# Kernel tuning notes

Measured on AMD Instinct MI355X. Metric: run time of the kernel, lower is better.

The kernel has to match this reference:

```python
import jax, jax.numpy as jnp
import numpy as np

B, C, H, W = 512, 2048, 8, 6
NATTR = 51
HID = 128
EPS = 1e-5


def setup_inputs() -> dict:
    key = jax.random.key(0)
    ks = jax.random.split(key, 12)
    inp = {
        "x_body_feat": jax.random.normal(ks[0], (B, C, H, W), dtype=jnp.float32),
        "x_face_feat": jax.random.normal(ks[1], (B, C, H, W), dtype=jnp.float32),
        "pose": jax.random.randint(ks[2], (B,), 0, 2, dtype=jnp.int64),
        "A_front": jax.random.normal(ks[3], (C, H, W), dtype=jnp.float32),
        # w1 MLP: Linear(2048->128), ReLU, Linear(128->2048), Sigmoid
        "W1": jax.random.normal(ks[4], (HID, C), dtype=jnp.float32) * (1.0 / np.sqrt(C)),
        "b1": jnp.zeros((HID,), dtype=jnp.float32),
        "W2": jax.random.normal(ks[5], (C, HID), dtype=jnp.float32) * (1.0 / np.sqrt(HID)),
        "b2": jnp.zeros((C,), dtype=jnp.float32),
        # logits: Linear(2048->nattr) + BatchNorm1d(nattr)
        "Wl": jax.random.normal(ks[6], (NATTR, C), dtype=jnp.float32) * (1.0 / np.sqrt(C)),
        "bl": jnp.zeros((NATTR,), dtype=jnp.float32),
        "gamma": jnp.ones((NATTR,), dtype=jnp.float32),
        "beta": jnp.zeros((NATTR,), dtype=jnp.float32),
    }
    return inp


def reference(x_body_feat, x_face_feat, pose, A_front, W1, b1, W2, b2, Wl, bl, gamma, beta):
    # Vectorized, mask-based form of the per-sample loop in A_operation.
    # comb_feat = body * A_front * face  -> [B, C, H, W]
    comb = x_body_feat * A_front[None] * x_face_feat
    # w1: MaxPool2d((8,6)) over full spatial extent -> [B, C], then MLP
    pooled = jnp.max(comb, axis=(2, 3))
    h = jax.nn.relu(pooled @ W1.T + b1)            # [B, 128]
    gate = jax.nn.sigmoid(h @ W2.T + b2)            # [B, 2048]
    cand = x_body_feat + gate[:, :, None, None]     # broadcast add, [B,C,H,W]
    # pose == 1 -> gated branch, else passthrough body features
    front = (pose == 1)[:, None, None, None]
    feat = jnp.where(front, cand, x_body_feat)
    # AdaptiveAvgPool2d(1) -> global mean
    gap = jnp.mean(feat, axis=(2, 3))               # [B, 2048]
    z = gap @ Wl.T + bl                             # [B, nattr]
    # BatchNorm1d in training mode: batch statistics (biased variance)
    mu = jnp.mean(z, axis=0)
    var = jnp.mean((z - mu) ** 2, axis=0)
    return gamma * (z - mu) * jax.lax.rsqrt(var + EPS) + beta
```

## Files before the change

### kernel.cpp

```cpp
#include <hip/hip_runtime.h>
#include <hip/hip_bf16.h>
#include <math.h>

#define B_    512
#define C_    2048
#define HW_   48
#define HID_  128
#define NATTR_ 51
#define EPS_  1e-5f

__global__ __launch_bounds__(256) void fused_pool(
    const float* __restrict__ body, const float* __restrict__ face,
    const float* __restrict__ A, float* __restrict__ pooled,
    float* __restrict__ bmean) {
  __shared__ float smax[256 * 13];
  __shared__ float ssum[256 * 13];
  const int t = threadIdx.x;
  const int base_f4 = blockIdx.x * 3072;
  const int cb12 = (blockIdx.x & 7) * 3072;
  const float4* __restrict__ b4 = (const float4*)body;
  const float4* __restrict__ f4 = (const float4*)face;
  const float4* __restrict__ a4 = (const float4*)A;
#pragma unroll
  for (int half = 0; half < 2; ++half) {
    float4 vb[6], vf[6], va[6];
#pragma unroll
    for (int j = 0; j < 6; ++j) {
      const int fl = t + 256 * (half * 6 + j);
      vb[j] = b4[base_f4 + fl];
      vf[j] = f4[base_f4 + fl];
      va[j] = a4[cb12 + fl];
    }
#pragma unroll
    for (int j = 0; j < 6; ++j) {
      const int fl = t + 256 * (half * 6 + j);
      const int rl = fl / 12, p = fl % 12;
      const float m0 = vb[j].x * va[j].x * vf[j].x;
      const float m1 = vb[j].y * va[j].y * vf[j].y;
      const float m2 = vb[j].z * va[j].z * vf[j].z;
      const float m3 = vb[j].w * va[j].w * vf[j].w;
      smax[rl * 13 + p] = fmaxf(fmaxf(m0, m1), fmaxf(m2, m3));
      ssum[rl * 13 + p] = (vb[j].x + vb[j].y) + (vb[j].z + vb[j].w);
    }
  }
  __syncthreads();
  float m = -INFINITY, s = 0.f;
#pragma unroll
  for (int p = 0; p < 12; ++p) {
    m = fmaxf(m, smax[t * 13 + p]);
    s += ssum[t * 13 + p];
  }
  const int row = blockIdx.x * 256 + t;
  pooled[row] = m;
  bmean[row] = s * (1.0f / 48.0f);
}

__global__ __launch_bounds__(256) void mlp1(
    const float* __restrict__ pooled, const float* __restrict__ W1,
    const float* __restrict__ b1, float* __restrict__ h) {
  const int t = threadIdx.x;
  const int lane = t & 63;
  const int w = t >> 6;
  const int sg = blockIdx.x >> 2;
  const int og = (blockIdx.x & 3) * 4 + w;
  const int s0 = sg * 8, o0 = og * 8;
  float acc[8][8] = {};
  const float* __restrict__ pb = pooled + lane;
  const float* __restrict__ wb = W1 + lane;
  for (int kc = 0; kc < 32; ++kc) {
    const int k = kc * 64;
    float p[8], wv[8];
#pragma unroll
    for (int i = 0; i < 8; ++i) p[i] = pb[(s0 + i) * C_ + k];
#pragma unroll
    for (int j = 0; j < 8; ++j) wv[j] = wb[(o0 + j) * C_ + k];
#pragma unroll
    for (int i = 0; i < 8; ++i)
#pragma unroll
      for (int j = 0; j < 8; ++j) acc[i][j] += p[i] * wv[j];
  }
#pragma unroll
  for (int d = 32; d >= 1; d >>= 1)
#pragma unroll
    for (int i = 0; i < 8; ++i)
#pragma unroll
      for (int j = 0; j < 8; ++j) acc[i][j] += __shfl_down(acc[i][j], d);
  if (lane == 0) {
#pragma unroll
    for (int i = 0; i < 8; ++i)
#pragma unroll
      for (int j = 0; j < 8; ++j)
        h[(s0 + i) * HID_ + o0 + j] = fmaxf(acc[i][j] + b1[o0 + j], 0.f);
  }
}

__global__ __launch_bounds__(256) void mlp2(
    const float* __restrict__ h, const float* __restrict__ W2,
    const float* __restrict__ b2, const float* __restrict__ bmean,
    const int* __restrict__ pose, float* __restrict__ gap) {
  extern __shared__ float w2s[];
  const int t = threadIdx.x;
  const int ct = blockIdx.x & 15, st = blockIdx.x >> 4;
  const int c0 = ct * 128, s_base = st * 32;
  const float4* __restrict__ wg = (const float4*)(W2 + c0 * HID_);
#pragma unroll
  for (int r = 0; r < 16; ++r) {
    const int f = t + 256 * r;
    const int row = f >> 5, col4 = f & 31;
    *(float4*)&w2s[row * 144 + col4 * 4] = wg[f];
  }
  __syncthreads();
  const int c_l = t & 127, sh = t >> 7;
  const int c = c0 + c_l;
  const float bias = b2[c];
  const float* __restrict__ wrow = &w2s[c_l * 144];
  for (int si = 0; si < 16; ++si) {
    const int s = s_base + sh * 16 + si;
    const float fr = (pose[s] == 1) ? 1.f : 0.f;
    float a0 = 0.f, a1 = 0.f, a2 = 0.f, a3 = 0.f;
#pragma unroll
    for (int j = 0; j < 32; ++j) {
      const float4 hv = *(const float4*)&h[s * HID_ + 4 * j];
      const float4 wv = *(const float4*)&wrow[4 * j];
      a0 += hv.x * wv.x;
      a1 += hv.y * wv.y;
      a2 += hv.z * wv.z;
      a3 += hv.w * wv.w;
    }
    const float acc = (a0 + a1) + (a2 + a3);
    const float g = 1.f / (1.f + expf(-(acc + bias)));
    gap[s * C_ + c] = bmean[s * C_ + c] + fr * g;
  }
}

__global__ __launch_bounds__(256) void logits_k(
    const float* __restrict__ gap, const float* __restrict__ Wl,
    const float* __restrict__ bl, float* __restrict__ z) {
  const int t = threadIdx.x;
  const int lane = t & 63;
  const int w = t >> 6;
  const int s0 = blockIdx.x * 4;
  const int o0 = w * 16;
  float acc[4][16] = {};
  const float* __restrict__ gb = gap + lane;
  const float* __restrict__ wb = Wl + lane;
  for (int kc = 0; kc < 32; ++kc) {
    const int k = kc * 64;
    float p[4], wv[16];
#pragma unroll
    for (int i = 0; i < 4; ++i) p[i] = gb[(s0 + i) * C_ + k];
#pragma unroll
    for (int j = 0; j < 16; ++j) {
      int o = o0 + j;
      if (o > NATTR_ - 1) o = NATTR_ - 1;
      wv[j] = wb[o * C_ + k];
    }
#pragma unroll
    for (int i = 0; i < 4; ++i)
#pragma unroll
      for (int j = 0; j < 16; ++j) acc[i][j] += p[i] * wv[j];
  }
#pragma unroll
  for (int d = 32; d >= 1; d >>= 1)
#pragma unroll
    for (int i = 0; i < 4; ++i)
#pragma unroll
      for (int j = 0; j < 16; ++j) acc[i][j] += __shfl_down(acc[i][j], d);
  if (lane == 0) {
#pragma unroll
    for (int i = 0; i < 4; ++i)
#pragma unroll
      for (int j = 0; j < 16; ++j) {
        const int o = o0 + j;
        if (o < NATTR_)
          z[(s0 + i) * NATTR_ + o] = acc[i][j] + bl[o];
      }
  }
}

__global__ __launch_bounds__(512) void bn_kernel(
    const float* __restrict__ z, const float* __restrict__ gamma,
    const float* __restrict__ beta, float* __restrict__ out) {
  const int c = blockIdx.x;
  const int t = threadIdx.x;
  const float v = z[t * NATTR_ + c];
  float a = v, b = v * v;
#pragma unroll
  for (int off = 32; off; off >>= 1) {
    a += __shfl_down(a, off);
    b += __shfl_down(b, off);
  }
  __shared__ float s1[8], s2[8];
  const int w = t >> 6;
  if ((t & 63) == 0) { s1[w] = a; s2[w] = b; }
  __syncthreads();
  __shared__ float mu_s, inv_s;
  if (t == 0) {
    float S = 0.f, Q = 0.f;
#pragma unroll
    for (int i = 0; i < 8; ++i) { S += s1[i]; Q += s2[i]; }
    const float m = S * (1.0f / B_);
    const float var = Q * (1.0f / B_) - m * m;
    mu_s = m;
    inv_s = 1.0f / sqrtf(var + EPS_);
  }
  __syncthreads();
  out[t * NATTR_ + c] = gamma[c] * (v - mu_s) * inv_s + beta[c];
}

extern "C" void kernel_launch(void* const* d_in, const int* in_sizes, int n_in,
                              void* d_out, int out_size, void* d_ws,
                              size_t ws_size, hipStream_t stream) {
  const float* body = (const float*)d_in[0];
  const float* face = (const float*)d_in[1];
  const int* pose = (const int*)d_in[2];
  const float* A = (const float*)d_in[3];
  const float* W1 = (const float*)d_in[4];
  const float* b1 = (const float*)d_in[5];
  const float* W2 = (const float*)d_in[6];
  const float* b2 = (const float*)d_in[7];
  const float* Wl = (const float*)d_in[8];
  const float* bl = (const float*)d_in[9];
  const float* gamma = (const float*)d_in[10];
  const float* beta = (const float*)d_in[11];
  float* out = (float*)d_out;

  float* ws = (float*)d_ws;
  float* pooled = ws;
  float* bmean = pooled + B_ * C_;
  float* h = bmean + B_ * C_;
  float* gap = h + B_ * HID_;
  float* z = gap + B_ * C_;

  fused_pool<<<dim3(4096), dim3(256), 0, stream>>>(body, face, A, pooled,
                                                   bmean);
  mlp1<<<dim3(256), dim3(256), 0, stream>>>(pooled, W1, b1, h);
  mlp2<<<dim3(256), dim3(256), 128 * 144 * 4, stream>>>(h, W2, b2, bmean,
                                                        pose, gap);
  logits_k<<<dim3(128), dim3(256), 0, stream>>>(gap, Wl, bl, z);
  bn_kernel<<<dim3(NATTR_), dim3(512), 0, stream>>>(z, gamma, beta, out);
}
```

Baseline: 505.8 us.

## Halve per-block work in pooling and GEMMs, add W2 transpose and nontemporal loads

The pooling kernel now covers 128 channel rows per block instead of 256, doubling the grid, and streams body and face through nontemporal loads. mlp1 and logits get smaller per-block tiles and twice as many blocks. mlp2 is rewritten to read a transposed W2 produced by a new transpose kernel, so loads are coalesced across channels and no shared-memory staging is needed. These changes aim to raise occupancy and improve memory access patterns, at the cost of one extra launch and less weight reuse per block.

```diff
diff --git a/kernel.cpp b/kernel.cpp
--- a/kernel.cpp
+++ b/kernel.cpp
@@ -9,31 +9,33 @@
 #define NATTR_ 51
 #define EPS_  1e-5f
 
+typedef float v4f __attribute__((ext_vector_type(4)));
+
 __global__ __launch_bounds__(256) void fused_pool(
     const float* __restrict__ body, const float* __restrict__ face,
     const float* __restrict__ A, float* __restrict__ pooled,
     float* __restrict__ bmean) {
-  __shared__ float smax[256 * 13];
-  __shared__ float ssum[256 * 13];
-  const int t = threadIdx.x;
-  const int base_f4 = blockIdx.x * 3072;
-  const int cb12 = (blockIdx.x & 7) * 3072;
-  const float4* __restrict__ b4 = (const float4*)body;
-  const float4* __restrict__ f4 = (const float4*)face;
-  const float4* __restrict__ a4 = (const float4*)A;
+  __shared__ float smax[128 * 13];
+  __shared__ float ssum[128 * 13];
+  const int t = threadIdx.x;
+  const int base_f4 = blockIdx.x * 1536;
+  const int a_base = (blockIdx.x & 15) * 1536;
+  const v4f* __restrict__ b4 = (const v4f*)body;
+  const v4f* __restrict__ f4 = (const v4f*)face;
+  const v4f* __restrict__ a4 = (const v4f*)A;
 #pragma unroll
   for (int half = 0; half < 2; ++half) {
-    float4 vb[6], vf[6], va[6];
-#pragma unroll
-    for (int j = 0; j < 6; ++j) {
-      const int fl = t + 256 * (half * 6 + j);
-      vb[j] = b4[base_f4 + fl];
-      vf[j] = f4[base_f4 + fl];
-      va[j] = a4[cb12 + fl];
-    }
-#pragma unroll
-    for (int j = 0; j < 6; ++j) {
-      const int fl = t + 256 * (half * 6 + j);
+    v4f vb[3], vf[3], va[3];
+#pragma unroll
+    for (int j = 0; j < 3; ++j) {
+      const int fl = t + 256 * (half * 3 + j);
+      vb[j] = __builtin_nontemporal_load(b4 + base_f4 + fl);
+      vf[j] = __builtin_nontemporal_load(f4 + base_f4 + fl);
+      va[j] = a4[a_base + fl];
+    }
+#pragma unroll
+    for (int j = 0; j < 3; ++j) {
+      const int fl = t + 256 * (half * 3 + j);
       const int rl = fl / 12, p = fl % 12;
       const float m0 = vb[j].x * va[j].x * vf[j].x;
       const float m1 = vb[j].y * va[j].y * vf[j].y;
@@ -44,15 +46,37 @@
     }
   }
   __syncthreads();
-  float m = -INFINITY, s = 0.f;
-#pragma unroll
-  for (int p = 0; p < 12; ++p) {
-    m = fmaxf(m, smax[t * 13 + p]);
-    s += ssum[t * 13 + p];
-  }
-  const int row = blockIdx.x * 256 + t;
-  pooled[row] = m;
-  bmean[row] = s * (1.0f / 48.0f);
+  if (t < 128) {
+    float m = -INFINITY, s = 0.f;
+#pragma unroll
+    for (int p = 0; p < 12; ++p) {
+      m = fmaxf(m, smax[t * 13 + p]);
+      s += ssum[t * 13 + p];
+    }
+    const int row = blockIdx.x * 128 + t;
+    pooled[row] = m;
+    bmean[row] = s * (1.0f / 48.0f);
+  }
+}
+
+__global__ __launch_bounds__(256) void w2t_kernel(
+    const float* __restrict__ W2, float* __restrict__ W2T) {
+  __shared__ float tile[64][65];
+  const int t = threadIdx.x;
+  const int kt = blockIdx.x & 1, ct = blockIdx.x >> 1;
+  const int c0 = ct * 64, k0 = kt * 64;
+  const int x = t & 63, y4 = t >> 6;
+#pragma unroll
+  for (int i = 0; i < 16; ++i) {
+    const int r = y4 + 4 * i;
+    tile[r][x] = W2[(c0 + r) * HID_ + k0 + x];
+  }
+  __syncthreads();
+#pragma unroll
+  for (int i = 0; i < 16; ++i) {
+    const int kk = y4 + 4 * i;
+    W2T[(k0 + kk) * C_ + c0 + x] = tile[x][kk];
+  }
 }
 
 __global__ __launch_bounds__(256) void mlp1(
@@ -61,74 +85,62 @@
   const int t = threadIdx.x;
   const int lane = t & 63;
   const int w = t >> 6;
-  const int sg = blockIdx.x >> 2;
-  const int og = (blockIdx.x & 3) * 4 + w;
-  const int s0 = sg * 8, o0 = og * 8;
-  float acc[8][8] = {};
+  const int s0 = (blockIdx.x >> 2) * 4;
+  const int o0 = ((blockIdx.x & 3) * 4 + w) * 8;
+  float acc[4][8] = {};
   const float* __restrict__ pb = pooled + lane;
   const float* __restrict__ wb = W1 + lane;
   for (int kc = 0; kc < 32; ++kc) {
     const int k = kc * 64;
-    float p[8], wv[8];
-#pragma unroll
-    for (int i = 0; i < 8; ++i) p[i] = pb[(s0 + i) * C_ + k];
+    float p[4], wv[8];
+#pragma unroll
+    for (int i = 0; i < 4; ++i) p[i] = pb[(s0 + i) * C_ + k];
 #pragma unroll
     for (int j = 0; j < 8; ++j) wv[j] = wb[(o0 + j) * C_ + k];
 #pragma unroll
-    for (int i = 0; i < 8; ++i)
+    for (int i = 0; i < 4; ++i)
 #pragma unroll
       for (int j = 0; j < 8; ++j) acc[i][j] += p[i] * wv[j];
   }
 #pragma unroll
   for (int d = 32; d >= 1; d >>= 1)
 #pragma unroll
-    for (int i = 0; i < 8; ++i)
+    for (int i = 0; i < 4; ++i)
 #pragma unroll
       for (int j = 0; j < 8; ++j) acc[i][j] += __shfl_down(acc[i][j], d);
   if (lane == 0) {
 #pragma unroll
-    for (int i = 0; i < 8; ++i)
+    for (int i = 0; i < 4; ++i)
 #pragma unroll
       for (int j = 0; j < 8; ++j)
         h[(s0 + i) * HID_ + o0 + j] = fmaxf(acc[i][j] + b1[o0 + j], 0.f);
   }
 }
 
-__global__ __launch_bounds__(256) void mlp2(
-    const float* __restrict__ h, const float* __restrict__ W2,
+__global__ __launch_bounds__(256) void mlp2_t(
+    const float* __restrict__ h, const float* __restrict__ W2T,
     const float* __restrict__ b2, const float* __restrict__ bmean,
     const int* __restrict__ pose, float* __restrict__ gap) {
-  extern __shared__ float w2s[];
-  const int t = threadIdx.x;
-  const int ct = blockIdx.x & 15, st = blockIdx.x >> 4;
-  const int c0 = ct * 128, s_base = st * 32;
-  const float4* __restrict__ wg = (const float4*)(W2 + c0 * HID_);
-#pragma unroll
-  for (int r = 0; r < 16; ++r) {
-    const int f = t + 256 * r;
-    const int row = f >> 5, col4 = f & 31;
-    *(float4*)&w2s[row * 144 + col4 * 4] = wg[f];
-  }
-  __syncthreads();
-  const int c_l = t & 127, sh = t >> 7;
-  const int c = c0 + c_l;
+  const int t = threadIdx.x;
+  const int c = (blockIdx.x & 7) * 256 + t;
+  const int s0 = (blockIdx.x >> 3) * 4;
+  float acc[4] = {};
+  for (int kq = 0; kq < 32; ++kq) {
+    float wv[4];
+#pragma unroll
+    for (int d = 0; d < 4; ++d) wv[d] = W2T[(4 * kq + d) * C_ + c];
+#pragma unroll
+    for (int i = 0; i < 4; ++i) {
+      const float4 hv = *(const float4*)&h[(s0 + i) * HID_ + 4 * kq];
+      acc[i] += hv.x * wv[0] + hv.y * wv[1] + hv.z * wv[2] + hv.w * wv[3];
+    }
+  }
   const float bias = b2[c];
-  const float* __restrict__ wrow = &w2s[c_l * 144];
-  for (int si = 0; si < 16; ++si) {
-    const int s = s_base + sh * 16 + si;
+#pragma unroll
+  for (int i = 0; i < 4; ++i) {
+    const int s = s0 + i;
     const float fr = (pose[s] == 1) ? 1.f : 0.f;
-    float a0 = 0.f, a1 = 0.f, a2 = 0.f, a3 = 0.f;
-#pragma unroll
-    for (int j = 0; j < 32; ++j) {
-      const float4 hv = *(const float4*)&h[s * HID_ + 4 * j];
-      const float4 wv = *(const float4*)&wrow[4 * j];
-      a0 += hv.x * wv.x;
-      a1 += hv.y * wv.y;
-      a2 += hv.z * wv.z;
-      a3 += hv.w * wv.w;
-    }
-    const float acc = (a0 + a1) + (a2 + a3);
-    const float g = 1.f / (1.f + expf(-(acc + bias)));
+    const float g = 1.f / (1.f + expf(-(acc[i] + bias)));
     gap[s * C_ + c] = bmean[s * C_ + c] + fr * g;
   }
 }
@@ -139,38 +151,38 @@
   const int t = threadIdx.x;
   const int lane = t & 63;
   const int w = t >> 6;
-  const int s0 = blockIdx.x * 4;
-  const int o0 = w * 16;
-  float acc[4][16] = {};
+  const int s0 = blockIdx.x * 2;
+  const int o0 = w * 13;
+  float acc[2][13] = {};
   const float* __restrict__ gb = gap + lane;
   const float* __restrict__ wb = Wl + lane;
   for (int kc = 0; kc < 32; ++kc) {
     const int k = kc * 64;
-    float p[4], wv[16];
-#pragma unroll
-    for (int i = 0; i < 4; ++i) p[i] = gb[(s0 + i) * C_ + k];
-#pragma unroll
-    for (int j = 0; j < 16; ++j) {
-      int o = o0 + j;
-      if (o > NATTR_ - 1) o = NATTR_ - 1;
-      wv[j] = wb[o * C_ + k];
-    }
-#pragma unroll
-    for (int i = 0; i < 4; ++i)
-#pragma unroll
-      for (int j = 0; j < 16; ++j) acc[i][j] += p[i] * wv[j];
+    float p[2], wv[13];
+#pragma unroll
+    for (int i = 0; i < 2; ++i) p[i] = gb[(s0 + i) * C_ + k];
+#pragma unroll
+    for (int j = 0; j < 13; ++j) {
+      const int o = o0 + j;
+      const int orow = (o < NATTR_) ? o : (NATTR_ - 1);
+      wv[j] = wb[orow * C_ + k];
+    }
+#pragma unroll
+    for (int i = 0; i < 2; ++i)
+#pragma unroll
+      for (int j = 0; j < 13; ++j) acc[i][j] += p[i] * wv[j];
   }
 #pragma unroll
   for (int d = 32; d >= 1; d >>= 1)
 #pragma unroll
-    for (int i = 0; i < 4; ++i)
-#pragma unroll
-      for (int j = 0; j < 16; ++j) acc[i][j] += __shfl_down(acc[i][j], d);
+    for (int i = 0; i < 2; ++i)
+#pragma unroll
+      for (int j = 0; j < 13; ++j) acc[i][j] += __shfl_down(acc[i][j], d);
   if (lane == 0) {
 #pragma unroll
-    for (int i = 0; i < 4; ++i)
-#pragma unroll
-      for (int j = 0; j < 16; ++j) {
+    for (int i = 0; i < 2; ++i)
+#pragma unroll
+      for (int j = 0; j < 13; ++j) {
         const int o = o0 + j;
         if (o < NATTR_)
           z[(s0 + i) * NATTR_ + o] = acc[i][j] + bl[o];
@@ -231,12 +243,13 @@
   float* h = bmean + B_ * C_;
   float* gap = h + B_ * HID_;
   float* z = gap + B_ * C_;
-
-  fused_pool<<<dim3(4096), dim3(256), 0, stream>>>(body, face, A, pooled,
+  float* W2T = z + B_ * NATTR_;
+
+  w2t_kernel<<<dim3(64), dim3(256), 0, stream>>>(W2, W2T);
+  fused_pool<<<dim3(8192), dim3(256), 0, stream>>>(body, face, A, pooled,
                                                    bmean);
-  mlp1<<<dim3(256), dim3(256), 0, stream>>>(pooled, W1, b1, h);
-  mlp2<<<dim3(256), dim3(256), 128 * 144 * 4, stream>>>(h, W2, b2, bmean,
-                                                        pose, gap);
-  logits_k<<<dim3(128), dim3(256), 0, stream>>>(gap, Wl, bl, z);
+  mlp1<<<dim3(512), dim3(256), 0, stream>>>(pooled, W1, b1, h);
+  mlp2_t<<<dim3(1024), dim3(256), 0, stream>>>(h, W2T, b2, bmean, pose, gap);
+  logits_k<<<dim3(256), dim3(256), 0, stream>>>(gap, Wl, bl, z);
   bn_kernel<<<dim3(NATTR_), dim3(512), 0, stream>>>(z, gamma, beta, out);
 }
```

After: 435.3 us. 13.9% less time.
